# Optimization experiments

Measured on AMD Instinct MI355X. Metric: run time of the kernel, lower is better.

The kernel has to match this reference:

```python
import jax, jax.numpy as jnp
import numpy as np

QUERY_DIM = 512
KEY_DIM = 512
NUM_HEADS = 16
HEAD_DIM = QUERY_DIM // NUM_HEADS


def setup_inputs() -> dict:
    key = jax.random.key(0)
    ks = jax.random.split(key, 10)
    B, T, S = 4, 2048, 2048
    s_q = 1.0 / np.sqrt(QUERY_DIM)
    s_k = 1.0 / np.sqrt(KEY_DIM)
    return {
        "x": jax.random.normal(ks[0], (B, T, QUERY_DIM), dtype=jnp.float32),
        "context": jax.random.normal(ks[1], (B, S, KEY_DIM), dtype=jnp.float32),
        "Wq": jax.random.normal(ks[2], (QUERY_DIM, QUERY_DIM), dtype=jnp.float32) * s_q,
        "bq": jnp.zeros((QUERY_DIM,), dtype=jnp.float32),
        "Wk": jax.random.normal(ks[3], (KEY_DIM, QUERY_DIM), dtype=jnp.float32) * s_k,
        "bk": jnp.zeros((QUERY_DIM,), dtype=jnp.float32),
        "Wv": jax.random.normal(ks[4], (KEY_DIM, QUERY_DIM), dtype=jnp.float32) * s_k,
        "bv": jnp.zeros((QUERY_DIM,), dtype=jnp.float32),
        "Wo": jax.random.normal(ks[5], (QUERY_DIM, QUERY_DIM), dtype=jnp.float32) * s_q,
        "bo": jnp.zeros((QUERY_DIM,), dtype=jnp.float32),
    }


def reference(x, context, Wq, bq, Wk, bk, Wv, bv, Wo, bo):
    B, T, C = x.shape
    S = context.shape[1]
    H, D = NUM_HEADS, HEAD_DIM
    scale = D ** -0.5
    # projections -> [B, H, T/S, D]
    q = (x @ Wq + bq).reshape(B, T, H, D).transpose(0, 2, 1, 3)
    k = (context @ Wk + bk).reshape(B, S, H, D).transpose(0, 2, 1, 3)
    v = (context @ Wv + bv).reshape(B, S, H, D).transpose(0, 2, 1, 3)
    # explicit attention matrix [B, H, T, S] (faithful to the unfused original)
    attn = jnp.einsum("bhtd,bhsd->bhts", q, k) * scale
    attn = jax.nn.softmax(attn, axis=-1)  # dropout is identity in eval mode
    out = jnp.einsum("bhts,bhsd->bhtd", attn, v)
    out = out.transpose(0, 2, 1, 3).reshape(B, T, C)
    return out @ Wo + bo
```

## Files before the change

kernel.cpp:

```cpp
#include <hip/hip_runtime.h>
#include <hip/hip_bf16.h>
#include <cmath>

typedef __bf16 bf16;
typedef __bf16 bf16x2 __attribute__((ext_vector_type(2)));
typedef __bf16 bf16x4 __attribute__((ext_vector_type(4)));
typedef __bf16 bf16x8 __attribute__((ext_vector_type(8)));
typedef float floatx4 __attribute__((ext_vector_type(4)));
typedef unsigned int uintx2 __attribute__((ext_vector_type(2)));
typedef unsigned int uintx4 __attribute__((ext_vector_type(4)));

#define MFMA_BF16(a, b, c) __builtin_amdgcn_mfma_f32_16x16x32_bf16((a), (b), (c), 0, 0, 0)

#if defined(__has_builtin)
#if __has_builtin(__builtin_amdgcn_global_load_lds)
#define HAVE_GLL 1
#endif
#if __has_builtin(__builtin_amdgcn_cvt_pk_bf16_f32)
#define HAVE_PKCVT 1
#endif
#if __has_builtin(__builtin_amdgcn_permlane32_swap) && __has_builtin(__builtin_amdgcn_permlane16_swap)
#define HAVE_PLSWAP 1
#endif
#endif

__device__ __forceinline__ void stage16(const bf16* g, bf16* ldsbase, int lane) {
#ifdef HAVE_GLL
    __builtin_amdgcn_global_load_lds((const __attribute__((address_space(1))) unsigned int*)g,
                                     (__attribute__((address_space(3))) unsigned int*)ldsbase,
                                     16, 0, 0);
#else
    *(int4*)(ldsbase + lane * 8) = *(const int4*)g;
#endif
}

__device__ __forceinline__ unsigned pk2(float a, float b) {
    bf16x2 t;
#ifdef HAVE_PKCVT
    t = __builtin_amdgcn_cvt_pk_bf16_f32(a, b);
#else
    t[0] = (bf16)a;
    t[1] = (bf16)b;
#endif
    return __builtin_bit_cast(unsigned, t);
}

__device__ __forceinline__ uintx2 p32swap(unsigned x, unsigned y) {
#ifdef HAVE_PLSWAP
    auto r = __builtin_amdgcn_permlane32_swap(x, y, false, false);
    uintx2 o;
    o[0] = r[0];
    o[1] = r[1];
    return o;
#else
    const int lane = threadIdx.x & 63;
    const unsigned px = __shfl(x, lane ^ 32);
    const unsigned py = __shfl(y, lane ^ 32);
    uintx2 o;
    o[0] = (lane & 32) ? py : x;
    o[1] = (lane & 32) ? y : px;
    return o;
#endif
}

__device__ __forceinline__ uintx2 p16swap(unsigned x, unsigned y) {
#ifdef HAVE_PLSWAP
    auto r = __builtin_amdgcn_permlane16_swap(x, y, false, false);
    uintx2 o;
    o[0] = r[0];
    o[1] = r[1];
    return o;
#else
    const int lane = threadIdx.x & 63;
    const unsigned px = __shfl(x, lane ^ 16);
    const unsigned py = __shfl(y, lane ^ 16);
    uintx2 o;
    o[0] = (lane & 16) ? py : x;
    o[1] = (lane & 16) ? y : px;
    return o;
#endif
}

__device__ __forceinline__ int detect_bf16(const void* x) {
    const unsigned short* u = (const unsigned short*)x;
    const int lane = threadIdx.x & 63;
    const unsigned short w0 = u[4 * lane], w1 = u[4 * lane + 2];
    const int e0 = (w0 >> 7) & 0xFF, e1 = (w1 >> 7) & 0xFF;
    const unsigned long long b0 = __ballot(e0 >= 96 && e0 <= 158);
    const unsigned long long b1 = __ballot(e1 >= 96 && e1 <= 158);
    return (__popcll(b0) + __popcll(b1)) >= 90;
}

struct PrepArgs {
    const void* x;
    const void* ctx;
    const void* W[4];
    const void* bias[4];
    bf16* xc;
    bf16* ctxc;
    bf16* WT[4];
    bf16* biasc;
};

__global__ __launch_bounds__(256) void prep(PrepArgs a) {
    const int tid = threadIdx.x;
    const int f = detect_bf16(a.x);
    const int bid = blockIdx.x;
    if (bid < 1024) {
        const int w = bid >> 8, tileid = bid & 255;
        const int bx = tileid & 15, by = tileid >> 4;
        const void* __restrict__ in = a.W[w];
        bf16* __restrict__ out = a.WT[w];
        __shared__ bf16 tile[32][33];
        const int tx = tid & 31, ty = tid >> 5;
        const int x = bx * 32 + tx;
        const int y0 = by * 32;
#pragma unroll
        for (int yy = ty; yy < 32; yy += 8) {
            const size_t idx = (size_t)(y0 + yy) * 512 + x;
            const float v = f ? (float)((const bf16*)in)[idx] : ((const float*)in)[idx];
            tile[yy][tx] = (bf16)v;
        }
        __syncthreads();
        const int xo = by * 32 + tx;
        const int y1 = bx * 32;
#pragma unroll
        for (int yy = ty; yy < 32; yy += 8)
            out[(size_t)(y1 + yy) * 512 + xo] = tile[tx][yy];
    } else if (bid < 5120) {
        if (f) return;
        const int seg = (bid >= 3072);
        const void* src = seg ? a.ctx : a.x;
        bf16* dst = seg ? a.ctxc : a.xc;
        const int off = (bid - (seg ? 3072 : 1024)) * 256 + tid;
        const float4 p = ((const float4*)src)[2 * off];
        const float4 q = ((const float4*)src)[2 * off + 1];
        bf16x8 o;
        o[0] = (bf16)p.x; o[1] = (bf16)p.y; o[2] = (bf16)p.z; o[3] = (bf16)p.w;
        o[4] = (bf16)q.x; o[5] = (bf16)q.y; o[6] = (bf16)q.z; o[7] = (bf16)q.w;
        *(bf16x8*)(dst + (size_t)off * 8) = o;
    } else {
        for (int e = tid; e < 2048; e += 256) {
            const int seg = e >> 9, off = e & 511;
            const float v =
                f ? (float)((const bf16*)a.bias[seg])[off] : ((const float*)a.bias[seg])[off];
            a.biasc[seg * 512 + off] = (bf16)v;
        }
    }
}

struct QkvArgs {
    const void* xraw;
    const void* ctxraw;
    const bf16* Aconv[3];
    const bf16* Wt[3];
    const bf16* bias;
    bf16* out[3];
    float scale[3];
};

__global__ __launch_bounds__(256) void gemm_qkv(QkvArgs a) {
    __shared__ __align__(16) bf16 lA[128 * 32];
    __shared__ __align__(16) bf16 lB[128 * 32];
    const int z = blockIdx.z;
    const int f = detect_bf16(a.xraw);
    const bf16* __restrict__ A =
        f ? (const bf16*)(z == 0 ? a.xraw : a.ctxraw) : a.Aconv[z];
    const bf16* __restrict__ Wt = a.Wt[z];
    const int tid = threadIdx.x, wave = tid >> 6, lane = tid & 63;
    const int qd = lane >> 4, j = lane & 15;
    const int m0 = blockIdx.x * 128, n0 = blockIdx.y * 128;
    const int wrow = (wave & 1) * 64, wcol = (wave >> 1) * 64;
    const int srow = wave * 16 + (lane >> 2);
    const int scol = (lane & 3) * 8;
    const bf16* agp = A + (size_t)(m0 + srow) * 512 + scol;
    const bf16* bgp = Wt + (size_t)(n0 + srow) * 512 + scol;
    bf16* lA0 = lA + wave * 512;
    bf16* lB0 = lB + wave * 512;

    floatx4 acc[4][4] = {};

    for (int k0 = 0; k0 < 512; k0 += 32) {
        stage16(agp + k0, lA0, lane);
        stage16(agp + k0 + (size_t)64 * 512, lA0 + 64 * 32, lane);
        stage16(bgp + k0, lB0, lane);
        stage16(bgp + k0 + (size_t)64 * 512, lB0 + 64 * 32, lane);
        __syncthreads();
        bf16x8 af[4], bfr[4];
#pragma unroll
        for (int i = 0; i < 4; ++i) {
            af[i] = *(const bf16x8*)(lA + (wrow + i * 16 + j) * 32 + qd * 8);
            bfr[i] = *(const bf16x8*)(lB + (wcol + i * 16 + j) * 32 + qd * 8);
        }
        if (z < 2) {
#pragma unroll
            for (int nt = 0; nt < 4; ++nt)
#pragma unroll
                for (int rf = 0; rf < 4; ++rf)
                    acc[nt][rf] = MFMA_BF16(bfr[nt], af[rf], acc[nt][rf]);
        } else {
#pragma unroll
            for (int rf = 0; rf < 4; ++rf)
#pragma unroll
                for (int nt = 0; nt < 4; ++nt)
                    acc[rf][nt] = MFMA_BF16(af[rf], bfr[nt], acc[rf][nt]);
        }
        __syncthreads();
    }

    const float scale = a.scale[z];
    const bf16* bias = a.bias + z * 512;
    bf16* __restrict__ C = a.out[z];
    if (z < 2) {
#pragma unroll
        for (int nt = 0; nt < 4; ++nt) {
            const int nb = n0 + wcol + nt * 16 + qd * 4;
            const bf16x4 bv4 = *(const bf16x4*)(bias + nb);
            const int h = nb >> 5, d0 = nb & 31;
#pragma unroll
            for (int rf = 0; rf < 4; ++rf) {
                const int m = m0 + wrow + rf * 16 + j;
                const int bb = m >> 11, t = m & 2047;
                bf16x4 pk;
#pragma unroll
                for (int r = 0; r < 4; ++r)
                    pk[r] = (bf16)((acc[nt][rf][r] + (float)bv4[r]) * scale);
                *(bf16x4*)(&C[(((size_t)bb * 16 + h) * 2048 + t) * 32 + d0]) = pk;
            }
        }
    } else {
#pragma unroll
        for (int nt = 0; nt < 4; ++nt) {
            const int n = n0 + wcol + nt * 16 + j;
            const float bv = (float)bias[n];
            const int h = n >> 5, d = n & 31;
#pragma unroll
            for (int rf = 0; rf < 4; ++rf) {
                const int t0 = m0 + wrow + rf * 16 + qd * 4;
                const int bb = t0 >> 11, s = t0 & 2047;
                bf16x4 pk;
#pragma unroll
                for (int r = 0; r < 4; ++r) pk[r] = (bf16)(acc[rf][nt][r] + bv);
                *(bf16x4*)(&C[(((size_t)bb * 16 + h) * 32 + d) * 2048 + s]) = pk;
            }
        }
    }
}

__global__ __launch_bounds__(256, 4) void attn_kernel(const bf16* __restrict__ Q,
                                                      const bf16* __restrict__ Kh,
                                                      const bf16* __restrict__ Vt,
                                                      bf16* __restrict__ O) {
    const int tid = threadIdx.x;
    const int wave = tid >> 6, lane = tid & 63;
    const int qd = lane >> 4, j = lane & 15;
    const int bh = blockIdx.x;
    const int b = bh >> 4, h = bh & 15;
    const int tw = blockIdx.y * 128 + wave * 32;

    const bf16* qbase = Q + ((size_t)bh * 2048 + tw) * 32;
    const bf16* kbase = Kh + (size_t)bh * 2048 * 32;
    const bf16* vbase = Vt + (size_t)bh * 32 * 2048;

    bf16x8 qf[2];
#pragma unroll
    for (int tf = 0; tf < 2; ++tf)
        qf[tf] = *(const bf16x8*)(qbase + (size_t)(tf * 16 + j) * 32 + qd * 8);

    bf16x8 ones;
#pragma unroll
    for (int e = 0; e < 8; ++e) ones[e] = (bf16)1.0f;

    const floatx4 zero = {0.f, 0.f, 0.f, 0.f};
    floatx4 oacc[2][2] = {};
    floatx4 dacc[2] = {};

    bf16x8 K0[4], K1[4], V0[4], V1[4];

    auto loadK = [&](int s0, bf16x8* k) {
#pragma unroll
        for (int sf = 0; sf < 4; ++sf)
            k[sf] = *(const bf16x8*)(kbase + (size_t)(s0 + sf * 16 + j) * 32 + qd * 8);
    };
    auto loadV = [&](int s0, bf16x8* v) {
#pragma unroll
        for (int dt = 0; dt < 2; ++dt)
#pragma unroll
            for (int kk = 0; kk < 2; ++kk)
                v[dt * 2 + kk] =
                    *(const bf16x8*)(vbase + (size_t)(dt * 16 + j) * 2048 + s0 + kk * 32 + qd * 8);
    };
    auto comp = [&](const bf16x8* kf, const bf16x8* vf) {
#pragma unroll
        for (int tf = 0; tf < 2; ++tf) {
            floatx4 sc[4];
#pragma unroll
            for (int sf = 0; sf < 4; ++sf) sc[sf] = MFMA_BF16(kf[sf], qf[tf], zero);
            unsigned SW[4][2];
#pragma unroll
            for (int sf = 0; sf < 4; ++sf) {
                const float e0 = __builtin_amdgcn_exp2f(sc[sf][0]);
                const float e1 = __builtin_amdgcn_exp2f(sc[sf][1]);
                const float e2 = __builtin_amdgcn_exp2f(sc[sf][2]);
                const float e3 = __builtin_amdgcn_exp2f(sc[sf][3]);
                SW[sf][0] = pk2(e0, e1);
                SW[sf][1] = pk2(e2, e3);
            }
            const uintx2 a0 = p32swap(SW[0][0], SW[1][0]);
            const uintx2 a1 = p32swap(SW[0][1], SW[1][1]);
            const uintx2 c0 = p32swap(SW[2][0], SW[3][0]);
            const uintx2 c1 = p32swap(SW[2][1], SW[3][1]);
            const uintx2 t0 = p16swap(a0[0], a0[1]);
            const uintx2 t1 = p16swap(a1[0], a1[1]);
            const uintx2 t2 = p16swap(c0[0], c0[1]);
            const uintx2 t3 = p16swap(c1[0], c1[1]);
            uintx4 w0, w1;
            w0[0] = t0[0]; w0[1] = t1[0]; w0[2] = t0[1]; w0[3] = t1[1];
            w1[0] = t2[0]; w1[1] = t3[0]; w1[2] = t2[1]; w1[3] = t3[1];
            const bf16x8 pf0 = __builtin_bit_cast(bf16x8, w0);
            const bf16x8 pf1 = __builtin_bit_cast(bf16x8, w1);
            oacc[tf][0] = MFMA_BF16(pf0, vf[0], oacc[tf][0]);
            oacc[tf][1] = MFMA_BF16(pf0, vf[2], oacc[tf][1]);
            dacc[tf] = MFMA_BF16(pf0, ones, dacc[tf]);
            oacc[tf][0] = MFMA_BF16(pf1, vf[1], oacc[tf][0]);
            oacc[tf][1] = MFMA_BF16(pf1, vf[3], oacc[tf][1]);
            dacc[tf] = MFMA_BF16(pf1, ones, dacc[tf]);
        }
    };

    loadK(0, K0);
    int s0 = 0;
    for (int it = 0; it < 15; ++it) {
        loadV(s0, V0);
        loadK(s0 + 64, K1);
        __builtin_amdgcn_sched_barrier(0);
        comp(K0, V0);
        loadV(s0 + 64, V1);
        loadK(s0 + 128, K0);
        __builtin_amdgcn_sched_barrier(0);
        comp(K1, V1);
        s0 += 128;
    }
    loadV(1920, V0);
    loadK(1984, K1);
    __builtin_amdgcn_sched_barrier(0);
    comp(K0, V0);
    loadV(1984, V1);
    __builtin_amdgcn_sched_barrier(0);
    comp(K1, V1);

#pragma unroll
    for (int tf = 0; tf < 2; ++tf)
#pragma unroll
        for (int r = 0; r < 4; ++r) {
            const float inv = 1.0f / dacc[tf][r];
            const int t = tw + tf * 16 + qd * 4 + r;
#pragma unroll
            for (int dt = 0; dt < 2; ++dt)
                O[((size_t)b * 2048 + t) * 512 + h * 32 + dt * 16 + j] =
                    (bf16)(oacc[tf][dt][r] * inv);
        }
}

__global__ __launch_bounds__(256) void gemm_out(const bf16* __restrict__ A,
                                                const bf16* __restrict__ Wt,
                                                const bf16* __restrict__ bias,
                                                void* __restrict__ C,
                                                const void* __restrict__ xraw) {
    __shared__ __align__(16) bf16 lA[128 * 32];
    __shared__ __align__(16) bf16 lB[128 * 32];
    const int oflag = detect_bf16(xraw);
    const int tid = threadIdx.x, wave = tid >> 6, lane = tid & 63;
    const int qd = lane >> 4, j = lane & 15;
    const int m0 = blockIdx.x * 128, n0 = blockIdx.y * 128;
    const int wrow = (wave & 1) * 64, wcol = (wave >> 1) * 64;
    const int srow = wave * 16 + (lane >> 2);
    const int scol = (lane & 3) * 8;
    const bf16* agp = A + (size_t)(m0 + srow) * 512 + scol;
    const bf16* bgp = Wt + (size_t)(n0 + srow) * 512 + scol;
    bf16* lA0 = lA + wave * 512;
    bf16* lB0 = lB + wave * 512;

    floatx4 acc[4][4] = {};

    for (int k0 = 0; k0 < 512; k0 += 32) {
        stage16(agp + k0, lA0, lane);
        stage16(agp + k0 + (size_t)64 * 512, lA0 + 64 * 32, lane);
        stage16(bgp + k0, lB0, lane);
        stage16(bgp + k0 + (size_t)64 * 512, lB0 + 64 * 32, lane);
        __syncthreads();
        bf16x8 af[4], bfr[4];
#pragma unroll
        for (int i = 0; i < 4; ++i) {
            af[i] = *(const bf16x8*)(lA + (wrow + i * 16 + j) * 32 + qd * 8);
            bfr[i] = *(const bf16x8*)(lB + (wcol + i * 16 + j) * 32 + qd * 8);
        }
#pragma unroll
        for (int nt = 0; nt < 4; ++nt)
#pragma unroll
            for (int rf = 0; rf < 4; ++rf)
                acc[nt][rf] = MFMA_BF16(bfr[nt], af[rf], acc[nt][rf]);
        __syncthreads();
    }

#pragma unroll
    for (int nt = 0; nt < 4; ++nt) {
        const int nb = n0 + wcol + nt * 16 + qd * 4;
        const bf16x4 bv4 = *(const bf16x4*)(bias + nb);
#pragma unroll
        for (int rf = 0; rf < 4; ++rf) {
            const int m = m0 + wrow + rf * 16 + j;
            if (oflag) {
                bf16x4 pk;
#pragma unroll
                for (int r = 0; r < 4; ++r) pk[r] = (bf16)(acc[nt][rf][r] + (float)bv4[r]);
                *(bf16x4*)((bf16*)C + (size_t)m * 512 + nb) = pk;
            } else {
                float4 v;
                v.x = acc[nt][rf][0] + (float)bv4[0];
                v.y = acc[nt][rf][1] + (float)bv4[1];
                v.z = acc[nt][rf][2] + (float)bv4[2];
                v.w = acc[nt][rf][3] + (float)bv4[3];
                *(float4*)((float*)C + (size_t)m * 512 + nb) = v;
            }
        }
    }
}

extern "C" void kernel_launch(void* const* d_in, const int* in_sizes, int n_in, void* d_out,
                              int out_size, void* d_ws, size_t ws_size, hipStream_t stream) {
    char* ws = (char*)d_ws;
    bf16* wqT = (bf16*)(ws + 1048576);
    bf16* wkT = (bf16*)(ws + 1572864);
    bf16* wvT = (bf16*)(ws + 2097152);
    bf16* woT = (bf16*)(ws + 2621440);
    bf16* biasc = (bf16*)(ws + 3145728);
    bf16* xc = (bf16*)(ws + 4194304);
    bf16* ctxc = (bf16*)(ws + 12582912);
    bf16* qws = (bf16*)(ws + 20971520);
    bf16* kws = (bf16*)(ws + 29360128);
    bf16* vtws = (bf16*)(ws + 37748736);
    bf16* aws = xc;

    PrepArgs pa;
    pa.x = d_in[0]; pa.ctx = d_in[1];
    pa.W[0] = d_in[2]; pa.W[1] = d_in[4]; pa.W[2] = d_in[6]; pa.W[3] = d_in[8];
    pa.bias[0] = d_in[3]; pa.bias[1] = d_in[5]; pa.bias[2] = d_in[7]; pa.bias[3] = d_in[9];
    pa.xc = xc; pa.ctxc = ctxc;
    pa.WT[0] = wqT; pa.WT[1] = wkT; pa.WT[2] = wvT; pa.WT[3] = woT;
    pa.biasc = biasc;
    prep<<<5121, 256, 0, stream>>>(pa);

    QkvArgs qa;
    qa.xraw = d_in[0]; qa.ctxraw = d_in[1];
    qa.Aconv[0] = xc; qa.Aconv[1] = ctxc; qa.Aconv[2] = ctxc;
    qa.Wt[0] = wqT; qa.Wt[1] = wkT; qa.Wt[2] = wvT;
    qa.bias = biasc;
    qa.out[0] = qws; qa.out[1] = kws; qa.out[2] = vtws;
    qa.scale[0] = 0.2550348593f; qa.scale[1] = 1.0f; qa.scale[2] = 1.0f;
    gemm_qkv<<<dim3(64, 4, 3), 256, 0, stream>>>(qa);

    attn_kernel<<<dim3(64, 16), 256, 0, stream>>>(qws, kws, vtws, aws);

    gemm_out<<<dim3(64, 4), 256, 0, stream>>>(aws, woT, biasc + 3 * 512, d_out, d_in[0]);
}
```

Baseline: 230.7 us.

## Use inline-asm global loads with explicit vmcnt waits in attention loop

Replaces the compiler-generated K/V/Q loads in the attention kernel with inline-asm global_load_dwordx4 using immediate offsets, and inserts explicit s_waitcnt vmcnt counts between the QK and PV phases. Compute is split so QK^T only waits on the K tile and PV waits on V, which is meant to let loads overlap more with MFMA work instead of blocking on all outstanding loads. V is now single-buffered and the loop is kept rolled. Hand-managed vmcnt counts are fragile: the compiler cannot see the asm loads, and any miscount can cause wrong data or extra stalls.

```diff
diff --git a/kernel.cpp b/kernel.cpp
--- a/kernel.cpp
+++ b/kernel.cpp
@@ -7,6 +7,7 @@
 typedef __bf16 bf16x4 __attribute__((ext_vector_type(4)));
 typedef __bf16 bf16x8 __attribute__((ext_vector_type(8)));
 typedef float floatx4 __attribute__((ext_vector_type(4)));
+typedef int intx4 __attribute__((ext_vector_type(4)));
 typedef unsigned int uintx2 __attribute__((ext_vector_type(2)));
 typedef unsigned int uintx4 __attribute__((ext_vector_type(4)));
 
@@ -33,6 +34,23 @@
     *(int4*)(ldsbase + lane * 8) = *(const int4*)g;
 #endif
 }
+
+__device__ __forceinline__ bf16x8 gload16(const bf16* p) {
+    intx4 r;
+    asm volatile("global_load_dwordx4 %0, %1, off" : "=v"(r) : "v"(p));
+    return __builtin_bit_cast(bf16x8, r);
+}
+template <int OFF>
+__device__ __forceinline__ bf16x8 gload16o(const bf16* p) {
+    intx4 r;
+    asm volatile("global_load_dwordx4 %0, %1, off offset:%2" : "=v"(r) : "v"(p), "n"(OFF));
+    return __builtin_bit_cast(bf16x8, r);
+}
+#define VMCNT(n)                                        \
+    do {                                                \
+        asm volatile("s_waitcnt vmcnt(" #n ")" ::);     \
+        __builtin_amdgcn_sched_barrier(0);              \
+    } while (0)
 
 __device__ __forceinline__ unsigned pk2(float a, float b) {
     bf16x2 t;
@@ -259,13 +277,33 @@
     const int tw = blockIdx.y * 128 + wave * 32;
 
     const bf16* qbase = Q + ((size_t)bh * 2048 + tw) * 32;
-    const bf16* kbase = Kh + (size_t)bh * 2048 * 32;
-    const bf16* vbase = Vt + (size_t)bh * 32 * 2048;
+    const bf16* kp = Kh + (size_t)bh * 2048 * 32 + (size_t)j * 32 + qd * 8;
+    const bf16* vp0 = Vt + (size_t)bh * 32 * 2048 + (size_t)j * 2048 + qd * 8;
+    const bf16* vp1 = vp0 + (size_t)16 * 2048;
 
     bf16x8 qf[2];
-#pragma unroll
-    for (int tf = 0; tf < 2; ++tf)
-        qf[tf] = *(const bf16x8*)(qbase + (size_t)(tf * 16 + j) * 32 + qd * 8);
+    qf[0] = gload16(qbase + (size_t)j * 32 + qd * 8);
+    qf[1] = gload16(qbase + (size_t)(16 + j) * 32 + qd * 8);
+
+    bf16x8 K0[4], K1[4], V[4];
+    auto loadK = [&](int s0, bf16x8* k) {
+        const bf16* p = kp + (size_t)s0 * 32;
+        k[0] = gload16o<0>(p);
+        k[1] = gload16o<1024>(p);
+        k[2] = gload16o<2048>(p);
+        k[3] = gload16o<3072>(p);
+    };
+    auto loadV = [&](int s0, bf16x8* v) {
+        const bf16* p0 = vp0 + s0;
+        const bf16* p1 = vp1 + s0;
+        v[0] = gload16o<0>(p0);
+        v[1] = gload16o<64>(p0);
+        v[2] = gload16o<0>(p1);
+        v[3] = gload16o<64>(p1);
+    };
+
+    loadK(0, K0);
+    VMCNT(4);
 
     bf16x8 ones;
 #pragma unroll
@@ -275,22 +313,7 @@
     floatx4 oacc[2][2] = {};
     floatx4 dacc[2] = {};
 
-    bf16x8 K0[4], K1[4], V0[4], V1[4];
-
-    auto loadK = [&](int s0, bf16x8* k) {
-#pragma unroll
-        for (int sf = 0; sf < 4; ++sf)
-            k[sf] = *(const bf16x8*)(kbase + (size_t)(s0 + sf * 16 + j) * 32 + qd * 8);
-    };
-    auto loadV = [&](int s0, bf16x8* v) {
-#pragma unroll
-        for (int dt = 0; dt < 2; ++dt)
-#pragma unroll
-            for (int kk = 0; kk < 2; ++kk)
-                v[dt * 2 + kk] =
-                    *(const bf16x8*)(vbase + (size_t)(dt * 16 + j) * 2048 + s0 + kk * 32 + qd * 8);
-    };
-    auto comp = [&](const bf16x8* kf, const bf16x8* vf) {
+    auto qk = [&](const bf16x8* kf, bf16x8* pf) {
 #pragma unroll
         for (int tf = 0; tf < 2; ++tf) {
             floatx4 sc[4];
@@ -317,37 +340,51 @@
             uintx4 w0, w1;
             w0[0] = t0[0]; w0[1] = t1[0]; w0[2] = t0[1]; w0[3] = t1[1];
             w1[0] = t2[0]; w1[1] = t3[0]; w1[2] = t2[1]; w1[3] = t3[1];
-            const bf16x8 pf0 = __builtin_bit_cast(bf16x8, w0);
-            const bf16x8 pf1 = __builtin_bit_cast(bf16x8, w1);
-            oacc[tf][0] = MFMA_BF16(pf0, vf[0], oacc[tf][0]);
-            oacc[tf][1] = MFMA_BF16(pf0, vf[2], oacc[tf][1]);
-            dacc[tf] = MFMA_BF16(pf0, ones, dacc[tf]);
-            oacc[tf][0] = MFMA_BF16(pf1, vf[1], oacc[tf][0]);
-            oacc[tf][1] = MFMA_BF16(pf1, vf[3], oacc[tf][1]);
-            dacc[tf] = MFMA_BF16(pf1, ones, dacc[tf]);
+            pf[tf * 2 + 0] = __builtin_bit_cast(bf16x8, w0);
+            pf[tf * 2 + 1] = __builtin_bit_cast(bf16x8, w1);
         }
     };
-
-    loadK(0, K0);
+    auto pv = [&](const bf16x8* vf, const bf16x8* pf) {
+#pragma unroll
+        for (int tf = 0; tf < 2; ++tf) {
+            oacc[tf][0] = MFMA_BF16(pf[tf * 2 + 0], vf[0], oacc[tf][0]);
+            oacc[tf][1] = MFMA_BF16(pf[tf * 2 + 0], vf[2], oacc[tf][1]);
+            dacc[tf] = MFMA_BF16(pf[tf * 2 + 0], ones, dacc[tf]);
+            oacc[tf][0] = MFMA_BF16(pf[tf * 2 + 1], vf[1], oacc[tf][0]);
+            oacc[tf][1] = MFMA_BF16(pf[tf * 2 + 1], vf[3], oacc[tf][1]);
+            dacc[tf] = MFMA_BF16(pf[tf * 2 + 1], ones, dacc[tf]);
+        }
+    };
+
+    bf16x8 pf[4];
     int s0 = 0;
+#pragma unroll 1
     for (int it = 0; it < 15; ++it) {
-        loadV(s0, V0);
+        loadV(s0, V);
         loadK(s0 + 64, K1);
-        __builtin_amdgcn_sched_barrier(0);
-        comp(K0, V0);
-        loadV(s0 + 64, V1);
+        VMCNT(8);
+        qk(K0, pf);
+        VMCNT(4);
+        pv(V, pf);
+        loadV(s0 + 64, V);
         loadK(s0 + 128, K0);
-        __builtin_amdgcn_sched_barrier(0);
-        comp(K1, V1);
+        VMCNT(8);
+        qk(K1, pf);
+        VMCNT(4);
+        pv(V, pf);
         s0 += 128;
     }
-    loadV(1920, V0);
+    loadV(1920, V);
     loadK(1984, K1);
-    __builtin_amdgcn_sched_barrier(0);
-    comp(K0, V0);
-    loadV(1984, V1);
-    __builtin_amdgcn_sched_barrier(0);
-    comp(K1, V1);
+    VMCNT(8);
+    qk(K0, pf);
+    VMCNT(4);
+    pv(V, pf);
+    loadV(1984, V);
+    VMCNT(4);
+    qk(K1, pf);
+    VMCNT(0);
+    pv(V, pf);
 
 #pragma unroll
     for (int tf = 0; tf < 2; ++tf)
```

New measurement: 231.3 us. Within noise of the previous version (+0.2%).
